# Optimization experiments

Hardware: AMD Instinct MI355X
Metric: run time of the kernel (lower is better)

## Reference

```python
import jax, jax.numpy as jnp
import numpy as np

N_E = 8192
E_DIM = 256
BETA = 0.25


def setup_inputs() -> dict:
    key = jax.random.key(0)
    k1, k2 = jax.random.split(key)
    z = jax.random.normal(k1, (16, 256, 32, 32), dtype=jnp.float32)
    # matches nn.Embedding weight init uniform_(-1/n_e, 1/n_e)
    embedding = jax.random.uniform(k2, (N_E, E_DIM), minval=-1.0 / N_E, maxval=1.0 / N_E, dtype=jnp.float32)
    return {"z": z, "embedding": embedding}


def reference(z, embedding):
    # (B,C,H,W) -> (B,H,W,C), flatten to (N, e_dim)
    zp = jnp.transpose(z, (0, 2, 3, 1))
    zf = zp.reshape(-1, E_DIM)
    # squared L2 distances to every codebook entry: (N, n_e)
    d = (jnp.sum(zf * zf, axis=1, keepdims=True)
         + jnp.sum(embedding * embedding, axis=1)
         - 2.0 * jnp.matmul(zf, embedding.T))
    idx = jnp.argmin(d, axis=1)  # (N,)
    # gather == one-hot @ embedding (same math, no dense one-hot)
    z_q = embedding[idx].reshape(zp.shape)  # (B,H,W,C)
    loss = (jnp.mean((jax.lax.stop_gradient(z_q) - zp) ** 2)
            + BETA * jnp.mean((z_q - jax.lax.stop_gradient(zp)) ** 2))
    # straight-through estimator
    z_q_st = zp + jax.lax.stop_gradient(z_q - zp)
    out = jnp.transpose(z_q_st, (0, 3, 1, 2))  # back to (B,C,H,W)
    min_encoding_indices = idx.reshape(zp.shape[:-1])  # (B,H,W)
    return out, loss, min_encoding_indices
```

## Files before the change

### kernel.cpp

```cpp
#include <hip/hip_runtime.h>
#include <hip/hip_bf16.h>

#define NROWS 16384
#define EDIM  256
#define NE    8192
#define OUT_N 4194304

typedef _Float16 v8h __attribute__((ext_vector_type(8)));
typedef _Float16 v4h __attribute__((ext_vector_type(4)));
typedef float    v4f __attribute__((ext_vector_type(4)));

#define OFF_S     0
#define OFF_E     16384
#define OFF_MARG  24576
#define OFF_IDX   40960
#define OFF_CH    57600
#define OFF_ZFH   1106176
#define OFF_EFH   3203328
#define OFF_LOSSP 4251904
#define WS_NEED_FLOATS 4252416

#define ESCALE   1048576.0f
#define DESCALE  0x1p-19f

static __device__ __forceinline__ unsigned short to_fp16_bits(float v) {
    _Float16 h = (_Float16)v;
    return __builtin_bit_cast(unsigned short, h);
}

__global__ __launch_bounds__(256) void k_pre(const float* __restrict__ z,
                                             const float* __restrict__ emb,
                                             float* __restrict__ ws) {
    float* S = ws + OFF_S;
    float* E = ws + OFF_E;
    float* MARG = ws + OFF_MARG;
    unsigned short* zfh = (unsigned short*)(ws + OFF_ZFH);
    unsigned short* efh = (unsigned short*)(ws + OFF_EFH);

    const int blk = blockIdx.x, tid = threadIdx.x;

    __shared__ float T[64][260];
    __shared__ double SD[64][4];
    __shared__ double AD[64][4];

    if (blk < 256) {
        const int r0 = blk * 64;
        const int b = r0 >> 10, hw0 = r0 & 1023;
        const int rr = tid & 63, kq = tid >> 6;
        const float* zp = z + (size_t)b * 262144 + hw0 + rr;
        double s = 0.0, a = 0.0;
#pragma unroll 8
        for (int kk = 0; kk < 64; ++kk) {
            int k = kq * 64 + kk;
            float v = zp[(size_t)k << 10];
            s += (double)v * (double)v;
            a += fabs((double)v);
            T[rr][k] = v;
        }
        SD[rr][kq] = s; AD[rr][kq] = a;
        __syncthreads();
        if (tid < 64) {
            double ss = SD[tid][0] + SD[tid][1] + SD[tid][2] + SD[tid][3];
            double aa = AD[tid][0] + AD[tid][1] + AD[tid][2] + AD[tid][3];
            S[r0 + tid] = (float)ss;
            MARG[r0 + tid] = 1.2e-4f + 6.5e-7f * (float)aa;
        }
        const int m = tid >> 2, koff = (tid & 3) * 64;
#pragma unroll
        for (int c = 0; c < 8; ++c) {
            unsigned short us[8];
#pragma unroll
            for (int j = 0; j < 8; ++j) us[j] = to_fp16_bits(T[m][koff + c * 8 + j]);
            *(uint4*)(zfh + (size_t)(r0 + m) * 256 + koff + c * 8) = *(uint4*)us;
        }
    } else {
        const int eb = blk - 256;
        const float* src = emb + (size_t)eb * 16384;
        unsigned short* dst = efh + (size_t)eb * 16384;
#pragma unroll
        for (int it = 0; it < 16; ++it) {
            int e4 = tid + it * 256;
            float4 v = ((const float4*)src)[e4];
            unsigned short us[4] = {to_fp16_bits(v.x * ESCALE), to_fp16_bits(v.y * ESCALE),
                                    to_fp16_bits(v.z * ESCALE), to_fp16_bits(v.w * ESCALE)};
            *(uint2*)(dst + (size_t)e4 * 4) = *(uint2*)us;
        }
        const int n0 = eb * 64;
        const int rr = tid & 63, kq = tid >> 6;
        const float* p = emb + (size_t)(n0 + rr) * 256 + kq * 64;
        double s = 0.0;
#pragma unroll 8
        for (int kk = 0; kk < 64; ++kk) { float v = p[kk]; s += (double)v * (double)v; }
        SD[rr][kq] = s;
        __syncthreads();
        if (tid < 64)
            E[n0 + tid] = (float)(SD[tid][0] + SD[tid][1] + SD[tid][2] + SD[tid][3]);
    }
}

__global__ __launch_bounds__(256) void k_gemm(
    const unsigned short* __restrict__ zfh, const unsigned short* __restrict__ efh,
    const float* __restrict__ S, const float* __restrict__ E,
    _Float16* __restrict__ CH) {
    __shared__ __align__(16) unsigned short As[128 * 64];
    __shared__ __align__(16) unsigned short Bs[128 * 64];

    const int tid = threadIdx.x;
    const int lane = tid & 63, wave = tid >> 6;
    const int wm = (wave & 1) * 64, wn = (wave >> 1) * 64;
    const int row0 = blockIdx.x * 128, col0 = blockIdx.y * 128;
    const int lm = lane & 15, lq = lane >> 4;

    v4f acc[4][4];
#pragma unroll
    for (int i = 0; i < 4; ++i)
#pragma unroll
        for (int j = 0; j < 4; ++j) acc[i][j] = (v4f){0.f, 0.f, 0.f, 0.f};

    for (int kt = 0; kt < 4; ++kt) {
        const int kbase = kt * 64;
#pragma unroll
        for (int it = 0; it < 4; ++it) {
            int e = tid + it * 256;
            int m = e >> 3, c = e & 7;
            uint4 va = *(const uint4*)(zfh + (size_t)(row0 + m) * 256 + kbase + c * 8);
            *(uint4*)(As + m * 64 + ((c ^ (m & 7)) << 3)) = va;
            uint4 vb = *(const uint4*)(efh + (size_t)(col0 + m) * 256 + kbase + c * 8);
            *(uint4*)(Bs + m * 64 + ((c ^ (m & 7)) << 3)) = vb;
        }
        __syncthreads();
#pragma unroll
        for (int s = 0; s < 2; ++s) {
            v8h af[4], bfr[4];
#pragma unroll
            for (int fi = 0; fi < 4; ++fi) {
                int m = wm + fi * 16 + lm;
                int c = (s << 2) | lq;
                af[fi] = *(const v8h*)(As + m * 64 + ((c ^ (m & 7)) << 3));
            }
#pragma unroll
            for (int fj = 0; fj < 4; ++fj) {
                int n = wn + fj * 16 + lm;
                int c = (s << 2) | lq;
                bfr[fj] = *(const v8h*)(Bs + n * 64 + ((c ^ (n & 7)) << 3));
            }
#pragma unroll
            for (int fi = 0; fi < 4; ++fi)
#pragma unroll
                for (int fj = 0; fj < 4; ++fj)
                    acc[fi][fj] = __builtin_amdgcn_mfma_f32_16x16x32_f16(
                        af[fi], bfr[fj], acc[fi][fj], 0, 0, 0);
        }
        __syncthreads();
    }

    float Sl[16];
#pragma unroll
    for (int fi = 0; fi < 4; ++fi)
#pragma unroll
        for (int r = 0; r < 4; ++r)
            Sl[fi * 4 + r] = S[row0 + wm + fi * 16 + lq * 4 + r];
    float En[4];
#pragma unroll
    for (int fj = 0; fj < 4; ++fj) En[fj] = E[col0 + wn + fj * 16 + lm];

    float dmin[16];
#pragma unroll
    for (int fi = 0; fi < 4; ++fi)
#pragma unroll
        for (int r = 0; r < 4; ++r) {
            float dm = __builtin_inff();
#pragma unroll
            for (int fj = 0; fj < 4; ++fj) {
                float d = (Sl[fi * 4 + r] + En[fj]) - acc[fi][fj][r] * DESCALE;
                dm = fminf(dm, d);
            }
            dmin[fi * 4 + r] = dm;
        }
#pragma unroll
    for (int msk = 1; msk < 16; msk <<= 1)
#pragma unroll
        for (int i = 0; i < 16; ++i)
            dmin[i] = fminf(dmin[i], __shfl_xor(dmin[i], msk, 64));

    if (lm == 0) {
        const int cb = blockIdx.y * 2 + (wn >> 6);
#pragma unroll
        for (int i = 0; i < 16; ++i) {
            int fi = i >> 2, r = i & 3;
            int gm = row0 + wm + fi * 16 + lq * 4 + r;
            float rel = dmin[i] - Sl[i];
            CH[(size_t)gm * 128 + cb] = (_Float16)rel;
        }
    }
}

__global__ __launch_bounds__(1024) void k_rescore(
    const float* __restrict__ z, const float* __restrict__ emb,
    const float* __restrict__ S, const float* __restrict__ E,
    const float* __restrict__ MARG, const unsigned short* __restrict__ efh,
    const _Float16* __restrict__ CH,
    int* __restrict__ IDX, float* __restrict__ idx_f) {
    __shared__ float zs[16][260];
    const int tid = threadIdx.x;
    const int r0 = blockIdx.x * 16;
    const int b = r0 >> 10, hw0 = r0 & 1023;
    {
        const int rr = tid & 15, kq = tid >> 4;
        const float* zp = z + (size_t)b * 262144 + hw0 + rr;
#pragma unroll
        for (int kk = 0; kk < 4; ++kk) {
            int k = kq * 4 + kk;
            zs[rr][k] = zp[(size_t)k << 10];
        }
    }
    __syncthreads();

    const int lane = tid & 63, wave = tid >> 6;
    const int rl = wave;
    const int r = r0 + rl;

    float m0 = (float)CH[(size_t)r * 128 + lane];
    float m1 = (float)CH[(size_t)r * 128 + 64 + lane];
    float g = fminf(m0, m1);
#pragma unroll
    for (int off = 32; off; off >>= 1) g = fminf(g, __shfl_xor(g, off, 64));
    const float thr = g + MARG[r];
    const float MB  = 0.75f * MARG[r];
    const float Sr = S[r];

    unsigned long long p0 = __ballot(m0 <= thr);
    unsigned long long p1 = __ballot(m1 <= thr);

    unsigned long long key = ~0ull;
    float grun = __builtin_inff();
    for (int half = 0; half < 2; ++half) {
        unsigned long long pm = half ? p1 : p0;
        while (pm) {
            int c = __ffsll((long long)pm) - 1; pm &= pm - 1;
            const int cb = half * 64 + c;
            const int j = (cb << 6) | lane;
            const unsigned short* eh = efh + ((size_t)j << 8);
            float macc = 0.0f;
#pragma unroll 8
            for (int k4 = 0; k4 < 64; ++k4) {
                v4h hv = *(const v4h*)(eh + k4 * 4);
                macc = fmaf(zs[rl][k4 * 4 + 0], (float)hv.x, macc);
                macc = fmaf(zs[rl][k4 * 4 + 1], (float)hv.y, macc);
                macc = fmaf(zs[rl][k4 * 4 + 2], (float)hv.z, macc);
                macc = fmaf(zs[rl][k4 * 4 + 3], (float)hv.w, macc);
            }
            float dref = (Sr + E[j]) - macc * DESCALE;
            float lmin = dref;
#pragma unroll
            for (int off = 32; off; off >>= 1) lmin = fminf(lmin, __shfl_xor(lmin, off, 64));
            grun = fminf(grun, lmin);
            unsigned long long sm = __ballot(dref <= grun + MB);
            while (sm) {
                int s = __ffsll((long long)sm) - 1; sm &= sm - 1;
                const int js = (cb << 6) | s;
                const float4* ep4 = (const float4*)(emb + ((size_t)js << 8));
                float m = 0.0f;
#pragma unroll 8
                for (int k4 = 0; k4 < 64; ++k4) {
                    float4 e4 = ep4[k4];
                    m = fmaf(zs[rl][k4 * 4 + 0], e4.x, m);
                    m = fmaf(zs[rl][k4 * 4 + 1], e4.y, m);
                    m = fmaf(zs[rl][k4 * 4 + 2], e4.z, m);
                    m = fmaf(zs[rl][k4 * 4 + 3], e4.w, m);
                }
                float d = (Sr + E[js]) - 2.0f * m;
                unsigned long long kk =
                    ((unsigned long long)__float_as_uint(d) << 32) | (unsigned)js;
                key = kk < key ? kk : key;
            }
        }
    }
    if (lane == 0) {
        int j = (int)(key & 0xFFFFFFFFull);
        IDX[r] = j;
        idx_f[r] = (float)j;
    }
}

__global__ __launch_bounds__(256) void k_out(const float* __restrict__ z,
                                             const float* __restrict__ emb,
                                             const int* __restrict__ idx,
                                             float* __restrict__ out,
                                             float* __restrict__ lossp) {
    __shared__ __align__(16) float EB[32 * 260];
    __shared__ float red[256];
    __shared__ int ids[32];
    const int tid = threadIdx.x;
    const int r0 = blockIdx.x * 32;
    const int b = r0 >> 10, hw0 = r0 & 1023;

    if (tid < 32) ids[tid] = idx[r0 + tid];
    __syncthreads();
#pragma unroll
    for (int it = 0; it < 8; ++it) {
        int i = tid + it * 256;
        int rr = i >> 6, k4 = i & 63;
        float4 v = *(const float4*)(emb + (size_t)ids[rr] * 256 + k4 * 4);
        *(float4*)(EB + rr * 260 + k4 * 4) = v;
    }
    __syncthreads();

    const float* zb = z + ((size_t)b << 18) + hw0;
    float*       ob = out + ((size_t)b << 18) + hw0;
    const int hq = tid & 7;
    const int cg = tid >> 3;
    float lsum = 0.0f;
#pragma unroll
    for (int it = 0; it < 8; ++it) {
        int c = it * 32 + cg;
        float4 zv = *(const float4*)(zb + (size_t)c * 1024 + hq * 4);
        float e0 = EB[(hq * 4 + 0) * 260 + c];
        float e1 = EB[(hq * 4 + 1) * 260 + c];
        float e2 = EB[(hq * 4 + 2) * 260 + c];
        float e3 = EB[(hq * 4 + 3) * 260 + c];
        float d0 = e0 - zv.x, d1 = e1 - zv.y, d2 = e2 - zv.z, d3 = e3 - zv.w;
        float4 ov = {zv.x + d0, zv.y + d1, zv.z + d2, zv.w + d3};
        *(float4*)(ob + (size_t)c * 1024 + hq * 4) = ov;
        lsum += d0 * d0 + d1 * d1 + d2 * d2 + d3 * d3;
    }
    red[tid] = lsum;
    __syncthreads();
    for (int off = 128; off; off >>= 1) {
        if (tid < off) red[tid] += red[tid + off];
        __syncthreads();
    }
    if (tid == 0) lossp[blockIdx.x] = red[0];
}

__global__ __launch_bounds__(256) void k_fin(const float* __restrict__ lossp,
                                             float* __restrict__ out_loss) {
    __shared__ float red[256];
    const int tid = threadIdx.x;
    red[tid] = lossp[tid] + lossp[tid + 256];
    __syncthreads();
    for (int off = 128; off; off >>= 1) {
        if (tid < off) red[tid] += red[tid + off];
        __syncthreads();
    }
    if (tid == 0) {
        float m = red[0] / 4194304.0f;
        out_loss[0] = m + 0.25f * m;
    }
}

#define FWS_S     0
#define FWS_E     (FWS_S + NROWS)
#define FWS_KEY   (FWS_E + NE)
#define FWS_IDX   (FWS_KEY + NROWS * 2)
#define FWS_LOSSP (FWS_IDX + NROWS)

__global__ void f_rowsum_z(const float* __restrict__ z, float* __restrict__ S) {
    int r = blockIdx.x * 256 + threadIdx.x;
    int b = r >> 10, hw = r & 1023;
    const float* p = z + (size_t)b * 262144 + hw;
    double s = 0.0;
#pragma unroll 8
    for (int c = 0; c < 256; ++c) { float v = p[(size_t)c * 1024]; s += (double)v * (double)v; }
    S[r] = (float)s;
}
__global__ void f_rowsum_e(const float* __restrict__ emb, float* __restrict__ E) {
    int row = blockIdx.x * 4 + (threadIdx.x >> 6);
    int lane = threadIdx.x & 63;
    const float* p = emb + (size_t)row * 256;
    double s = 0.0;
#pragma unroll
    for (int i = 0; i < 4; ++i) { float v = p[lane + i * 64]; s += (double)v * (double)v; }
    for (int off = 32; off; off >>= 1) s += __shfl_down(s, off, 64);
    if (lane == 0) E[row] = (float)s;
}
__global__ __launch_bounds__(256, 4) void f_gemm_argmin(
    const float* __restrict__ z, const float* __restrict__ emb,
    const float* __restrict__ S, const float* __restrict__ E,
    unsigned long long* __restrict__ keys) {
    __shared__ __align__(16) float As[32][128];
    __shared__ __align__(16) float Bs[32][133];
    const int tid = threadIdx.x;
    const int tx = tid & 15, ty = tid >> 4;
    const int row0 = blockIdx.x * 128, col0 = blockIdx.y * 128;
    const int b = row0 >> 10, hw0 = row0 & 1023;
    const float* zb = z + (size_t)b * 262144 + hw0;
    float acc[8][8];
#pragma unroll
    for (int i = 0; i < 8; ++i)
#pragma unroll
        for (int j = 0; j < 8; ++j) acc[i][j] = 0.0f;
    for (int kt = 0; kt < 8; ++kt) {
        const int kbase = kt * 32;
#pragma unroll
        for (int it = 0; it < 4; ++it) {
            int e = tid + it * 256;
            int k = e >> 5, m4 = (e & 31) << 2;
            *(float4*)&As[k][m4] = *(const float4*)(zb + (size_t)(kbase + k) * 1024 + m4);
        }
#pragma unroll
        for (int it = 0; it < 4; ++it) {
            int e = tid + it * 256;
            int n = e >> 3, k4 = (e & 7) << 2;
            float4 v = *(const float4*)(emb + (size_t)(col0 + n) * 256 + kbase + k4);
            Bs[k4 + 0][n] = v.x; Bs[k4 + 1][n] = v.y;
            Bs[k4 + 2][n] = v.z; Bs[k4 + 3][n] = v.w;
        }
        __syncthreads();
#pragma unroll 8
        for (int k = 0; k < 32; ++k) {
            float4 a0 = *(const float4*)&As[k][tx * 4];
            float4 a1 = *(const float4*)&As[k][64 + tx * 4];
            float4 b0 = *(const float4*)&Bs[k][ty * 4];
            float4 b1 = *(const float4*)&Bs[k][64 + ty * 4];
            float a_[8] = {a0.x, a0.y, a0.z, a0.w, a1.x, a1.y, a1.z, a1.w};
            float b_[8] = {b0.x, b0.y, b0.z, b0.w, b1.x, b1.y, b1.z, b1.w};
#pragma unroll
            for (int i = 0; i < 8; ++i)
#pragma unroll
                for (int j = 0; j < 8; ++j) acc[i][j] += a_[i] * b_[j];
        }
        __syncthreads();
    }
    float4 S0 = *(const float4*)(S + row0 + tx * 4);
    float4 S1 = *(const float4*)(S + row0 + 64 + tx * 4);
    float4 E0 = *(const float4*)(E + col0 + ty * 4);
    float4 E1 = *(const float4*)(E + col0 + 64 + ty * 4);
    float Sr[8] = {S0.x, S0.y, S0.z, S0.w, S1.x, S1.y, S1.z, S1.w};
    float Ec[8] = {E0.x, E0.y, E0.z, E0.w, E1.x, E1.y, E1.z, E1.w};
    unsigned long long best[8];
#pragma unroll
    for (int i = 0; i < 8; ++i) best[i] = ~0ull;
#pragma unroll
    for (int j = 0; j < 8; ++j) {
        int col = col0 + ((j < 4) ? (ty * 4 + j) : (64 + ty * 4 + j - 4));
#pragma unroll
        for (int i = 0; i < 8; ++i) {
            float t = Sr[i] + Ec[j];
            float d = t - 2.0f * acc[i][j];
            unsigned ud = __float_as_uint(d);
            ud = (ud & 0x80000000u) ? ~ud : (ud | 0x80000000u);
            unsigned long long key = ((unsigned long long)ud << 32) | (unsigned)col;
            if (key < best[i]) best[i] = key;
        }
    }
    __syncthreads();
    unsigned long long* Sk = (unsigned long long*)&As[0][0];
#pragma unroll
    for (int i = 0; i < 4; ++i) {
        Sk[ty * 128 + tx * 4 + i] = best[i];
        Sk[ty * 128 + 64 + tx * 4 + i] = best[4 + i];
    }
    __syncthreads();
    if (tid < 128) {
        unsigned long long m = ~0ull;
#pragma unroll
        for (int t = 0; t < 16; ++t) {
            unsigned long long v = Sk[t * 128 + tid];
            m = v < m ? v : m;
        }
        atomicMin(&keys[row0 + tid], m);
    }
}
__global__ void f_merge(const unsigned long long* __restrict__ keys,
                        int* __restrict__ idx, float* __restrict__ idx_f) {
    int r = blockIdx.x * 256 + threadIdx.x;
    int bestj = (int)(keys[r] & 0xFFFFFFFFull);
    idx[r] = bestj;
    idx_f[r] = (float)bestj;
}

extern "C" void kernel_launch(void* const* d_in, const int* in_sizes, int n_in,
                              void* d_out, int out_size, void* d_ws, size_t ws_size,
                              hipStream_t stream) {
    const float* z   = (const float*)d_in[0];
    const float* emb = (const float*)d_in[1];
    float* out = (float*)d_out;
    float* ws  = (float*)d_ws;

    if (ws_size >= (size_t)WS_NEED_FLOATS * 4) {
        float* S = ws + OFF_S;
        float* E = ws + OFF_E;
        float* MARG = ws + OFF_MARG;
        int* IDX = (int*)(ws + OFF_IDX);
        _Float16* CH = (_Float16*)(ws + OFF_CH);
        unsigned short* ZFH = (unsigned short*)(ws + OFF_ZFH);
        unsigned short* EFH = (unsigned short*)(ws + OFF_EFH);
        float* LOSSP = ws + OFF_LOSSP;

        k_pre<<<384, 256, 0, stream>>>(z, emb, ws);
        dim3 g(NROWS / 128, NE / 128);
        k_gemm<<<g, 256, 0, stream>>>(ZFH, EFH, S, E, CH);
        k_rescore<<<NROWS / 16, 1024, 0, stream>>>(z, emb, S, E, MARG, EFH, CH,
                                                   IDX, out + OUT_N + 1);
        k_out<<<NROWS / 32, 256, 0, stream>>>(z, emb, IDX, out, LOSSP);
        k_fin<<<1, 256, 0, stream>>>(LOSSP, out + OUT_N);
    } else {
        float* S = ws + FWS_S;
        float* E = ws + FWS_E;
        unsigned long long* KEYS = (unsigned long long*)(ws + FWS_KEY);
        int* IDX = (int*)(ws + FWS_IDX);
        float* LOSSP = ws + FWS_LOSSP;

        f_rowsum_z<<<NROWS / 256, 256, 0, stream>>>(z, S);
        f_rowsum_e<<<NE / 4, 256, 0, stream>>>(emb, E);
        hipMemsetAsync(KEYS, 0xFF, NROWS * sizeof(unsigned long long), stream);
        dim3 g(NROWS / 128, NE / 128);
        f_gemm_argmin<<<g, 256, 0, stream>>>(z, emb, S, E, KEYS);
        f_merge<<<NROWS / 256, 256, 0, stream>>>(KEYS, IDX, out + OUT_N + 1);
        k_out<<<NROWS / 32, 256, 0, stream>>>(z, emb, IDX, out, LOSSP);
        k_fin<<<1, 256, 0, stream>>>(LOSSP, out + OUT_N);
    }
}
```

Measured before the change: 333.2 us.

## Rescore with fp16 z rows from workspace and lazy fp32 z via shuffles

The rescore kernel now runs 4 rows per 256-thread block instead of 16 per 1024-thread block. It reads each row's pre-converted fp16 z from workspace into a small shared tile rather than gathering the strided fp32 z into shared memory. The fp16 coarse dot uses 8-wide vector loads of both operands. The exact fp32 rescore loads z lazily into registers only when needed and broadcasts it via wave shuffles. This removes the strided global gather and block-wide sync, but adds shuffle overhead to the exact path and relies on the fp16 z scaling matching the previous fp32 path.

```diff
diff --git a/kernel.cpp b/kernel.cpp
--- a/kernel.cpp
+++ b/kernel.cpp
@@ -195,30 +195,21 @@
     }
 }
 
-__global__ __launch_bounds__(1024) void k_rescore(
+__global__ __launch_bounds__(256) void k_rescore(
     const float* __restrict__ z, const float* __restrict__ emb,
     const float* __restrict__ S, const float* __restrict__ E,
-    const float* __restrict__ MARG, const unsigned short* __restrict__ efh,
+    const float* __restrict__ MARG,
+    const unsigned short* __restrict__ zfh,
+    const unsigned short* __restrict__ efh,
     const _Float16* __restrict__ CH,
     int* __restrict__ IDX, float* __restrict__ idx_f) {
-    __shared__ float zs[16][260];
+    __shared__ _Float16 zh[4][264];
     const int tid = threadIdx.x;
-    const int r0 = blockIdx.x * 16;
-    const int b = r0 >> 10, hw0 = r0 & 1023;
-    {
-        const int rr = tid & 15, kq = tid >> 4;
-        const float* zp = z + (size_t)b * 262144 + hw0 + rr;
-#pragma unroll
-        for (int kk = 0; kk < 4; ++kk) {
-            int k = kq * 4 + kk;
-            zs[rr][k] = zp[(size_t)k << 10];
-        }
-    }
-    __syncthreads();
-
     const int lane = tid & 63, wave = tid >> 6;
-    const int rl = wave;
-    const int r = r0 + rl;
+    const int r = blockIdx.x * 4 + wave;
+    const int b = r >> 10, hw = r & 1023;
+
+    *(uint2*)&zh[wave][lane * 4] = *(const uint2*)(zfh + (size_t)r * 256 + lane * 4);
 
     float m0 = (float)CH[(size_t)r * 128 + lane];
     float m1 = (float)CH[(size_t)r * 128 + 64 + lane];
@@ -232,23 +223,27 @@
     unsigned long long p0 = __ballot(m0 <= thr);
     unsigned long long p1 = __ballot(m1 <= thr);
 
+    float zreg[4];
+    bool zld = false;
+
     unsigned long long key = ~0ull;
     float grun = __builtin_inff();
+    const v8h* zhp = (const v8h*)&zh[wave][0];
     for (int half = 0; half < 2; ++half) {
         unsigned long long pm = half ? p1 : p0;
         while (pm) {
             int c = __ffsll((long long)pm) - 1; pm &= pm - 1;
             const int cb = half * 64 + c;
             const int j = (cb << 6) | lane;
-            const unsigned short* eh = efh + ((size_t)j << 8);
+            const v8h* ehp = (const v8h*)(efh + ((size_t)j << 8));
             float macc = 0.0f;
 #pragma unroll 8
-            for (int k4 = 0; k4 < 64; ++k4) {
-                v4h hv = *(const v4h*)(eh + k4 * 4);
-                macc = fmaf(zs[rl][k4 * 4 + 0], (float)hv.x, macc);
-                macc = fmaf(zs[rl][k4 * 4 + 1], (float)hv.y, macc);
-                macc = fmaf(zs[rl][k4 * 4 + 2], (float)hv.z, macc);
-                macc = fmaf(zs[rl][k4 * 4 + 3], (float)hv.w, macc);
+            for (int k8 = 0; k8 < 32; ++k8) {
+                v8h ev = ehp[k8];
+                v8h zv = zhp[k8];
+#pragma unroll
+                for (int i = 0; i < 8; ++i)
+                    macc = fmaf((float)zv[i], (float)ev[i], macc);
             }
             float dref = (Sr + E[j]) - macc * DESCALE;
             float lmin = dref;
@@ -259,15 +254,25 @@
             while (sm) {
                 int s = __ffsll((long long)sm) - 1; sm &= sm - 1;
                 const int js = (cb << 6) | s;
+                if (!zld) {
+#pragma unroll
+                    for (int t = 0; t < 4; ++t)
+                        zreg[t] = z[(size_t)b * 262144 +
+                                    (size_t)(lane + 64 * t) * 1024 + hw];
+                    zld = true;
+                }
                 const float4* ep4 = (const float4*)(emb + ((size_t)js << 8));
                 float m = 0.0f;
 #pragma unroll 8
                 for (int k4 = 0; k4 < 64; ++k4) {
                     float4 e4 = ep4[k4];
-                    m = fmaf(zs[rl][k4 * 4 + 0], e4.x, m);
-                    m = fmaf(zs[rl][k4 * 4 + 1], e4.y, m);
-                    m = fmaf(zs[rl][k4 * 4 + 2], e4.z, m);
-                    m = fmaf(zs[rl][k4 * 4 + 3], e4.w, m);
+                    int t = k4 >> 4;
+#pragma unroll
+                    for (int i = 0; i < 4; ++i) {
+                        float zk = __shfl(zreg[t], (k4 * 4 + i) & 63, 64);
+                        float ek = (i == 0) ? e4.x : (i == 1) ? e4.y : (i == 2) ? e4.z : e4.w;
+                        m = fmaf(zk, ek, m);
+                    }
                 }
                 float d = (Sr + E[js]) - 2.0f * m;
                 unsigned long long kk =
@@ -491,8 +496,8 @@
         k_pre<<<384, 256, 0, stream>>>(z, emb, ws);
         dim3 g(NROWS / 128, NE / 128);
         k_gemm<<<g, 256, 0, stream>>>(ZFH, EFH, S, E, CH);
-        k_rescore<<<NROWS / 16, 1024, 0, stream>>>(z, emb, S, E, MARG, EFH, CH,
-                                                   IDX, out + OUT_N + 1);
+        k_rescore<<<NROWS / 4, 256, 0, stream>>>(z, emb, S, E, MARG, ZFH, EFH, CH,
+                                                 IDX, out + OUT_N + 1);
         k_out<<<NROWS / 32, 256, 0, stream>>>(z, emb, IDX, out, LOSSP);
         k_fin<<<1, 256, 0, stream>>>(LOSSP, out + OUT_N);
     } else {
```

Measured after the change: 358.1 us. +7.5%, slower.
